# Kernel optimization log

Measured on AMD Instinct MI355X. Metric: run time of the kernel, lower is better.

## Reference

```python
import jax, jax.numpy as jnp
import numpy as np

N_NODES = 100_000
N_INC = 400_000
N_EDGES = 20_000
N_GRAPHS = 512
N_SEQ = 16
SEQ_LEN = 32
F_IN = 128
HIDDEN = 256
HEADS = 4
OUT = HIDDEN // HEADS  # 64 per head, concat -> HIDDEN
RNN_H = 256
OUT_DIM = 128
NEG_SLOPE = 0.2


def setup_inputs() -> dict:
    key = jax.random.key(0)
    ks = jax.random.split(key, 20)
    p = lambda i, shape: jax.random.normal(ks[i], shape, jnp.float32) * 0.05
    return {
        "x": jax.random.normal(ks[0], (N_NODES, F_IN), jnp.float32),
        "he_node": jax.random.randint(ks[1], (N_INC,), 0, N_NODES),
        "he_edge": jax.random.randint(ks[2], (N_INC,), 0, N_EDGES),
        "batch": jnp.sort(jax.random.randint(ks[3], (N_NODES,), 0, N_GRAPHS)),
        "w_lin": p(4, (F_IN, HIDDEN)),
        "att": p(5, (HEADS, 2 * OUT)),
        "bias": p(6, (HIDDEN,)),
        "w_ih0": p(7, (2, 4 * RNN_H, HIDDEN)),
        "w_hh0": p(8, (2, 4 * RNN_H, RNN_H)),
        "b_ih0": p(9, (2, 4 * RNN_H)),
        "b_hh0": p(10, (2, 4 * RNN_H)),
        "w_ih1": p(11, (2, 4 * RNN_H, 2 * RNN_H)),
        "w_hh1": p(12, (2, 4 * RNN_H, RNN_H)),
        "b_ih1": p(13, (2, 4 * RNN_H)),
        "b_hh1": p(14, (2, 4 * RNN_H)),
        "w_causal": p(15, (2 * RNN_H, HIDDEN)),
        "b_causal": p(16, (HIDDEN,)),
        "w_link": p(17, (HIDDEN, OUT_DIM)),
        "b_link": p(18, (OUT_DIM,)),
    }


def _segment_softmax(logits, seg, num_segments):
    m = jax.ops.segment_max(logits, seg, num_segments)
    m = jnp.where(jnp.isfinite(m), m, 0.0)
    e = jnp.exp(logits - m[seg])
    s = jax.ops.segment_sum(e, seg, num_segments)
    return e / jnp.maximum(s[seg], 1e-16)


def hypergraph_conv(x, he_node, he_edge, w_lin, att, bias):
    # PyG HypergraphConv, use_attention=True, attention_mode='node'.
    xh = (x @ w_lin).reshape(-1, HEADS, OUT)  # [N,H,O]
    ones_inc = jnp.ones((N_INC,), x.dtype)
    cnt_e = jax.ops.segment_sum(ones_inc, he_edge, N_EDGES)  # hyperedge sizes
    # hyperedge_attr = mean of incident raw node features, then shared lin
    eattr = jax.ops.segment_sum(x[he_node], he_edge, N_EDGES) / jnp.maximum(cnt_e, 1.0)[:, None]
    eh = (eattr @ w_lin).reshape(-1, HEADS, OUT)  # [M,H,O]
    x_i = xh[he_node]  # [E,H,O]
    e_j = eh[he_edge]  # [E,H,O]
    alpha = jnp.einsum("ehd,hd->eh", jnp.concatenate([x_i, e_j], axis=-1), att)
    alpha = jax.nn.leaky_relu(alpha, NEG_SLOPE)
    alpha = _segment_softmax(alpha, he_edge, N_EDGES)  # softmax within each hyperedge
    Binv = jnp.where(cnt_e > 0, 1.0 / cnt_e, 0.0)  # hyperedge degree norm
    deg = jax.ops.segment_sum(ones_inc, he_node, N_NODES)
    Dinv = jnp.where(deg > 0, 1.0 / deg, 0.0)  # node degree norm
    # node -> hyperedge, then hyperedge -> node, attention applied both hops
    out_e = Binv[:, None, None] * jax.ops.segment_sum(alpha[:, :, None] * x_i, he_edge, N_EDGES)
    out_n = Dinv[:, None, None] * jax.ops.segment_sum(alpha[:, :, None] * out_e[he_edge], he_node, N_NODES)
    return out_n.reshape(-1, HIDDEN) + bias


def _lstm_dir(xs, w_ih, w_hh, b_ih, b_hh, reverse):
    # xs: [T,B,I]; torch gate order i,f,g,o
    B = xs.shape[1]
    H = w_hh.shape[1]
    def step(carry, x_t):
        h, c = carry
        g = x_t @ w_ih.T + h @ w_hh.T + b_ih + b_hh
        i, f, gg, o = jnp.split(g, 4, axis=-1)
        c = jax.nn.sigmoid(f) * c + jax.nn.sigmoid(i) * jnp.tanh(gg)
        h = jax.nn.sigmoid(o) * jnp.tanh(c)
        return (h, c), h
    h0 = jnp.zeros((B, H), xs.dtype)
    _, hs = jax.lax.scan(step, (h0, h0), xs, reverse=reverse)
    return hs


def bilstm(x_seq, w_ih, w_hh, b_ih, b_hh):
    xs = jnp.swapaxes(x_seq, 0, 1)  # [T,B,I]
    fwd = _lstm_dir(xs, w_ih[0], w_hh[0], b_ih[0], b_hh[0], False)
    bwd = _lstm_dir(xs, w_ih[1], w_hh[1], b_ih[1], b_hh[1], True)
    return jnp.swapaxes(jnp.concatenate([fwd, bwd], axis=-1), 0, 1)


def reference(x, he_node, he_edge, batch, w_lin, att, bias,
              w_ih0, w_hh0, b_ih0, b_hh0, w_ih1, w_hh1, b_ih1, b_hh1,
              w_causal, b_causal, w_link, b_link):
    h = jax.nn.relu(hypergraph_conv(x, he_node, he_edge, w_lin, att, bias))  # [N,HIDDEN]
    cnt_g = jax.ops.segment_sum(jnp.ones((N_NODES,), h.dtype), batch, N_GRAPHS)
    pooled = jax.ops.segment_sum(h, batch, N_GRAPHS) / jnp.maximum(cnt_g, 1.0)[:, None]
    seq = pooled.reshape(N_SEQ, SEQ_LEN, HIDDEN)  # equal-length sequences of graphs
    l1 = bilstm(seq, w_ih0, w_hh0, b_ih0, b_hh0)   # [S,T,2*RNN_H]
    l2 = bilstm(l1, w_ih1, w_hh1, b_ih1, b_hh1)
    causal = jax.nn.relu(l2 @ w_causal + b_causal)
    return jax.nn.sigmoid(causal @ w_link + b_link)  # [S,T,OUT_DIM]
```

## Files before the change

### kernel.cpp

```cpp
#include <hip/hip_runtime.h>
#include <math.h>

#define N_NODES  100000
#define N_INC    400000
#define N_EDGES  20000
#define N_GRAPHS 512
#define F_IN     128
#define HID      256
#define RNN_H    256
#define ODIM     128

__global__ void k_count(const int* __restrict__ he_node, const int* __restrict__ he_edge,
                        int* __restrict__ cnt_e, int* __restrict__ deg) {
  int i = blockIdx.x * 256 + threadIdx.x;
  if (i >= N_INC) return;
  atomicAdd(&cnt_e[he_edge[i]], 1);
  atomicAdd(&deg[he_node[i]], 1);
}

__global__ __launch_bounds__(1024)
void k_scan(const int* __restrict__ cnt, int* __restrict__ start, int n) {
  __shared__ int part[1024];
  int tid = threadIdx.x;
  int chunk = (n + 1023) / 1024;
  int lo = tid * chunk; if (lo > n) lo = n;
  int hi = lo + chunk;  if (hi > n) hi = n;
  int s = 0;
  for (int i = lo; i < hi; ++i) s += cnt[i];
  part[tid] = s;
  __syncthreads();
  for (int off = 1; off < 1024; off <<= 1) {
    int v = (tid >= off) ? part[tid - off] : 0;
    __syncthreads();
    part[tid] += v;
    __syncthreads();
  }
  int run = (tid == 0) ? 0 : part[tid - 1];
  for (int i = lo; i < hi; ++i) { start[i] = run; run += cnt[i]; }
  if (tid == 1023) start[n] = part[1023];
}

__global__ void k_fill(const int* __restrict__ he_node, const int* __restrict__ he_edge,
                       const int* __restrict__ e_start, const int* __restrict__ n_start,
                       int* __restrict__ cur_e, int* __restrict__ cur_n,
                       int* __restrict__ e_idx, int* __restrict__ n_idx) {
  int i = blockIdx.x * 256 + threadIdx.x;
  if (i >= N_INC) return;
  int e = he_edge[i]; int p = atomicAdd(&cur_e[e], 1); e_idx[e_start[e] + p] = i;
  int nn = he_node[i]; int q = atomicAdd(&cur_n[nn], 1); n_idx[n_start[nn] + q] = i;
}

__global__ void k_transpose(const float* __restrict__ in, float* __restrict__ out,
                            int rows, int cols) {
  int idx = blockIdx.x * 256 + threadIdx.x;
  if (idx >= rows * cols) return;
  int r = idx / cols, c = idx - r * cols;
  out[c * rows + r] = in[idx];
}

template<int TT, int TR>
__global__ __launch_bounds__(256)
void k_gemm(const float* __restrict__ A, const float* __restrict__ WT,
            float* __restrict__ C, int M, int N, int K,
            const float* __restrict__ bias1, const float* __restrict__ bias2,
            int act, int remap) {
  __shared__ float As[TT][64];
  __shared__ float Ws[TT][64];
  const int m0 = blockIdx.y * TT, n0 = blockIdx.x * TT;
  const int tid = threadIdx.x;
  const int tc = tid & 15, tr = tid >> 4;
  float acc[TR][TR];
#pragma unroll
  for (int r = 0; r < TR; ++r)
#pragma unroll
    for (int c = 0; c < TR; ++c) acc[r][c] = 0.f;

  for (int kc = 0; kc < K; kc += 64) {
    for (int it = tid; it < TT * 16; it += 256) {
      int r = it >> 4, c4 = it & 15;
      int sw = ((c4 ^ (r >> 3)) & 15) << 2;
      int row = m0 + r;
      float4 v = {0.f, 0.f, 0.f, 0.f};
      if (row < M) v = *(const float4*)&A[(size_t)row * K + kc + c4 * 4];
      *(float4*)&As[r][sw] = v;
      float4 wv = *(const float4*)&WT[(size_t)(n0 + r) * K + kc + c4 * 4];
      *(float4*)&Ws[r][sw] = wv;
    }
    __syncthreads();
#pragma unroll 4
    for (int k4 = 0; k4 < 16; ++k4) {
      float4 wv[TR], av[TR];
#pragma unroll
      for (int c = 0; c < TR; ++c) {
        int rw = tc * TR + c;
        wv[c] = *(const float4*)&Ws[rw][((k4 ^ (rw >> 3)) & 15) << 2];
      }
#pragma unroll
      for (int r = 0; r < TR; ++r) {
        int ra = tr * TR + r;
        av[r] = *(const float4*)&As[ra][((k4 ^ (ra >> 3)) & 15) << 2];
      }
#pragma unroll
      for (int r = 0; r < TR; ++r)
#pragma unroll
        for (int c = 0; c < TR; ++c)
          acc[r][c] += av[r].x * wv[c].x + av[r].y * wv[c].y +
                       av[r].z * wv[c].z + av[r].w * wv[c].w;
    }
    __syncthreads();
  }

#pragma unroll
  for (int r = 0; r < TR; ++r) {
    int row = m0 + tr * TR + r;
    if (row >= M) continue;
    int orow = remap ? ((row & 15) * 32 + (row >> 4)) : row;
#pragma unroll
    for (int c4 = 0; c4 < TR; c4 += 4) {
      float4 o;
      float* op = &o.x;
#pragma unroll
      for (int c = 0; c < 4; ++c) {
        int col = n0 + tc * TR + c4 + c;
        float v = acc[r][c4 + c] +
                  (bias1 ? bias1[col] : 0.f) + (bias2 ? bias2[col] : 0.f);
        if (act == 1) v = fmaxf(v, 0.f);
        else if (act == 2) v = 1.f / (1.f + expf(-v));
        op[c] = v;
      }
      *(float4*)&C[(size_t)orow * N + n0 + tc * TR + c4] = o;
    }
  }
}

__global__ __launch_bounds__(256)
void k_eattr(const float* __restrict__ x, const int* __restrict__ he_node,
             const int* __restrict__ e_start, const int* __restrict__ e_idx,
             float* __restrict__ eattr) {
  int m = blockIdx.x * 4 + (threadIdx.x >> 6);
  if (m >= N_EDGES) return;
  int lane = threadIdx.x & 63;
  int c4 = lane & 31, jp = lane >> 5;
  int begin = e_start[m], end = e_start[m + 1];
  float4 acc = {0.f, 0.f, 0.f, 0.f};
  for (int j = begin + jp; j < end; j += 2) {
    float4 v = *(const float4*)&x[(size_t)he_node[e_idx[j]] * F_IN + c4 * 4];
    acc.x += v.x; acc.y += v.y; acc.z += v.z; acc.w += v.w;
  }
  acc.x += __shfl_xor(acc.x, 32); acc.y += __shfl_xor(acc.y, 32);
  acc.z += __shfl_xor(acc.z, 32); acc.w += __shfl_xor(acc.w, 32);
  if (jp == 0) {
    float inv = 1.f / fmaxf((float)(end - begin), 1.f);
    float4 o = {acc.x * inv, acc.y * inv, acc.z * inv, acc.w * inv};
    *(float4*)&eattr[(size_t)m * F_IN + c4 * 4] = o;
  }
}

__global__ __launch_bounds__(256)
void k_dot(const float* __restrict__ X, const float* __restrict__ att,
           float* __restrict__ s, int half, int nrows) {
  int row = blockIdx.x * 4 + (threadIdx.x >> 6);
  if (row >= nrows) return;
  int lane = threadIdx.x & 63;
  int h = lane >> 4;
  float4 v = *(const float4*)&X[(size_t)row * HID + lane * 4];
  float4 a = *(const float4*)&att[h * 128 + half * 64 + (lane & 15) * 4];
  float p = v.x * a.x + v.y * a.y + v.z * a.z + v.w * a.w;
  p += __shfl_xor(p, 1); p += __shfl_xor(p, 2);
  p += __shfl_xor(p, 4); p += __shfl_xor(p, 8);
  if ((lane & 15) == 0) s[(size_t)row * 4 + h] = p;
}

__global__ void k_logit(const int* __restrict__ he_node, const int* __restrict__ he_edge,
                        const float* __restrict__ s_n, const float* __restrict__ s_e,
                        float* __restrict__ alpha) {
  int i = blockIdx.x * 256 + threadIdx.x;
  if (i >= N_INC) return;
  float4 a = *(const float4*)&s_n[(size_t)he_node[i] * 4];
  float4 b = *(const float4*)&s_e[(size_t)he_edge[i] * 4];
  float4 o;
  o.x = a.x + b.x; o.y = a.y + b.y; o.z = a.z + b.z; o.w = a.w + b.w;
  o.x = o.x > 0.f ? o.x : 0.2f * o.x;
  o.y = o.y > 0.f ? o.y : 0.2f * o.y;
  o.z = o.z > 0.f ? o.z : 0.2f * o.z;
  o.w = o.w > 0.f ? o.w : 0.2f * o.w;
  *(float4*)&alpha[(size_t)i * 4] = o;
}

__global__ __launch_bounds__(256)
void k_softmax(const int* __restrict__ e_start, const int* __restrict__ e_idx,
               float* __restrict__ alpha) {
  int m = blockIdx.x * 4 + (threadIdx.x >> 6);
  if (m >= N_EDGES) return;
  int lane = threadIdx.x & 63;
  int begin = e_start[m], end = e_start[m + 1];
  int cnt = end - begin;
  if (cnt == 0) return;
  int nch = (cnt + 63) >> 6;
  float mx[4] = {-1e30f, -1e30f, -1e30f, -1e30f};
  for (int ch = 0; ch < nch; ++ch) {
    int j = begin + ch * 64 + lane;
    if (j < end) {
      float4 a = *(const float4*)&alpha[(size_t)e_idx[j] * 4];
      mx[0] = fmaxf(mx[0], a.x); mx[1] = fmaxf(mx[1], a.y);
      mx[2] = fmaxf(mx[2], a.z); mx[3] = fmaxf(mx[3], a.w);
    }
  }
#pragma unroll
  for (int h = 0; h < 4; ++h)
    for (int off = 32; off; off >>= 1) mx[h] = fmaxf(mx[h], __shfl_xor(mx[h], off));
  float s[4] = {0.f, 0.f, 0.f, 0.f};
  for (int ch = 0; ch < nch; ++ch) {
    int j = begin + ch * 64 + lane;
    if (j < end) {
      int i = e_idx[j];
      float4 a = *(const float4*)&alpha[(size_t)i * 4];
      a.x = expf(a.x - mx[0]); a.y = expf(a.y - mx[1]);
      a.z = expf(a.z - mx[2]); a.w = expf(a.w - mx[3]);
      *(float4*)&alpha[(size_t)i * 4] = a;
      s[0] += a.x; s[1] += a.y; s[2] += a.z; s[3] += a.w;
    }
  }
#pragma unroll
  for (int h = 0; h < 4; ++h) {
    for (int off = 32; off; off >>= 1) s[h] += __shfl_xor(s[h], off);
    s[h] = 1.f / fmaxf(s[h], 1e-16f);
  }
  for (int ch = 0; ch < nch; ++ch) {
    int j = begin + ch * 64 + lane;
    if (j < end) {
      int i = e_idx[j];
      float4 a = *(const float4*)&alpha[(size_t)i * 4];
      a.x *= s[0]; a.y *= s[1]; a.z *= s[2]; a.w *= s[3];
      *(float4*)&alpha[(size_t)i * 4] = a;
    }
  }
}

__global__ __launch_bounds__(256)
void k_out_e(const float* __restrict__ xh, const float* __restrict__ alpha,
             const int* __restrict__ e_start, const int* __restrict__ e_idx,
             const int* __restrict__ he_node, float* __restrict__ out_e) {
  int m = blockIdx.x * 4 + (threadIdx.x >> 6);
  if (m >= N_EDGES) return;
  int lane = threadIdx.x & 63, h = lane >> 4;
  int begin = e_start[m], end = e_start[m + 1];
  float4 acc = {0.f, 0.f, 0.f, 0.f};
  for (int j = begin; j < end; ++j) {
    int i = e_idx[j];
    float a = alpha[(size_t)i * 4 + h];
    float4 v = *(const float4*)&xh[(size_t)he_node[i] * HID + lane * 4];
    acc.x += a * v.x; acc.y += a * v.y; acc.z += a * v.z; acc.w += a * v.w;
  }
  float bi = (end > begin) ? 1.f / (float)(end - begin) : 0.f;
  float4 o = {acc.x * bi, acc.y * bi, acc.z * bi, acc.w * bi};
  *(float4*)&out_e[(size_t)m * HID + lane * 4] = o;
}

__global__ __launch_bounds__(256)
void k_out_n(const float* __restrict__ out_e, const float* __restrict__ alpha,
             const int* __restrict__ n_start, const int* __restrict__ n_idx,
             const int* __restrict__ he_edge, const float* __restrict__ bias,
             float* __restrict__ hout) {
  int n = blockIdx.x * 4 + (threadIdx.x >> 6);
  if (n >= N_NODES) return;
  int lane = threadIdx.x & 63, h = lane >> 4;
  int begin = n_start[n], end = n_start[n + 1];
  float4 acc = {0.f, 0.f, 0.f, 0.f};
  for (int j = begin; j < end; ++j) {
    int i = n_idx[j];
    float a = alpha[(size_t)i * 4 + h];
    float4 v = *(const float4*)&out_e[(size_t)he_edge[i] * HID + lane * 4];
    acc.x += a * v.x; acc.y += a * v.y; acc.z += a * v.z; acc.w += a * v.w;
  }
  float di = (end > begin) ? 1.f / (float)(end - begin) : 0.f;
  float4 bb = *(const float4*)&bias[lane * 4];
  float4 o;
  o.x = fmaxf(acc.x * di + bb.x, 0.f);
  o.y = fmaxf(acc.y * di + bb.y, 0.f);
  o.z = fmaxf(acc.z * di + bb.z, 0.f);
  o.w = fmaxf(acc.w * di + bb.w, 0.f);
  *(float4*)&hout[(size_t)n * HID + lane * 4] = o;
}

__global__ void k_gstart(const int* __restrict__ batch, int* __restrict__ gs) {
  int g = blockIdx.x * 256 + threadIdx.x;
  if (g > N_GRAPHS) return;
  int lo = 0, hi = N_NODES;
  while (lo < hi) { int mid = (lo + hi) >> 1; if (batch[mid] < g) lo = mid + 1; else hi = mid; }
  gs[g] = lo;
}

__global__ __launch_bounds__(256)
void k_pool(const float* __restrict__ h, const int* __restrict__ gs,
            float* __restrict__ pooled) {
  __shared__ float4 part[4][64];
  int g = blockIdx.x, tid = threadIdx.x;
  int rs = tid >> 6, c4 = tid & 63;
  int begin = gs[g], end = gs[g + 1];
  float4 acc = {0.f, 0.f, 0.f, 0.f};
  for (int n = begin + rs; n < end; n += 4) {
    float4 v = *(const float4*)&h[(size_t)n * HID + c4 * 4];
    acc.x += v.x; acc.y += v.y; acc.z += v.z; acc.w += v.w;
  }
  part[rs][c4] = acc;
  __syncthreads();
  if (rs == 0) {
    float4 a = part[0][c4], b = part[1][c4], c = part[2][c4], d = part[3][c4];
    float inv = 1.f / fmaxf((float)(end - begin), 1.f);
    float4 o = {(a.x + b.x + c.x + d.x) * inv, (a.y + b.y + c.y + d.y) * inv,
                (a.z + b.z + c.z + d.z) * inv, (a.w + b.w + c.w + d.w) * inv};
    *(float4*)&pooled[(size_t)g * HID + c4 * 4] = o;
  }
}

__global__ __launch_bounds__(256)
void k_lstm2(const float* __restrict__ xg, const float* __restrict__ w_hh,
             float* __restrict__ out, float* __restrict__ hbuf,
             int* __restrict__ stamp, int rst, int rsb) {
  __shared__ float4 ws4[64][64];
  __shared__ float4 hs[16 * 64];
  const int dir = blockIdx.x >> 4, q = blockIdx.x & 15;
  const int tid = threadIdx.x;
  const int l = tid & 63, w = tid >> 6;
  const int ks = l & 3, rg = l >> 2;

  for (int it = tid; it < 4096; it += 256) {
    int row = it >> 6, c4 = it & 63;
    int g = row >> 4, r = row & 15;
    float4 v = *(const float4*)&w_hh[((size_t)dir * 1024 + g * 256 + q * 16 + r) * 256 + c4 * 4];
    ws4[row][c4 ^ ((c4 >> 4) & 3) ^ (r & 7)] = v;
  }
  __syncthreads();

  float cst[4] = {0.f, 0.f, 0.f, 0.f};
  for (int t = 0; t < 32; ++t) {
    const int te = dir ? (31 - t) : t;
    float xr[4][4];
#pragma unroll
    for (int lb = 0; lb < 4; ++lb) {
      const float* xp = &xg[(size_t)((w * 4 + lb) * rsb + te * rst) * 2048 + dir * 1024 + q * 16 + rg];
      xr[0][lb] = xp[0];
      xr[1][lb] = xp[256];
      xr[2][lb] = xp[512];
      xr[3][lb] = xp[768];
    }
    if (t > 0) {
      for (;;) {
        int sv = t;
        if (l < 16)
          sv = __hip_atomic_load(&stamp[dir * 16 + l], __ATOMIC_RELAXED, __HIP_MEMORY_SCOPE_AGENT);
        if (__all(sv >= t)) break;
        __builtin_amdgcn_s_sleep(1);
      }
    }
    const float* hprev = hbuf + ((size_t)(t & 1) * 2 + dir) * 16 * 256;
    float4 hv0, hv1, hv2, hv3;
    {
      const float* a0 = hprev + (0 * 256 + tid) * 4;
      const float* a1 = hprev + (1 * 256 + tid) * 4;
      const float* a2 = hprev + (2 * 256 + tid) * 4;
      const float* a3 = hprev + (3 * 256 + tid) * 4;
      asm volatile(
        "global_load_dwordx4 %0, %4, off sc0 sc1\n"
        "global_load_dwordx4 %1, %5, off sc0 sc1\n"
        "global_load_dwordx4 %2, %6, off sc0 sc1\n"
        "global_load_dwordx4 %3, %7, off sc0 sc1\n"
        "s_waitcnt vmcnt(0)"
        : "=&v"(hv0), "=&v"(hv1), "=&v"(hv2), "=&v"(hv3)
        : "v"(a0), "v"(a1), "v"(a2), "v"(a3)
        : "memory");
    }
#pragma unroll
    for (int i = 0; i < 4; ++i) {
      int idx = i * 256 + tid;
      int b = idx >> 6, cc = idx & 63;
      float4 hv = (i == 0) ? hv0 : (i == 1) ? hv1 : (i == 2) ? hv2 : hv3;
      hs[b * 64 + (cc ^ ((cc >> 4) & 3))] = hv;
    }
    __syncthreads();

    float acc[4][4];
#pragma unroll
    for (int g = 0; g < 4; ++g)
#pragma unroll
      for (int lb = 0; lb < 4; ++lb) acc[g][lb] = 0.f;
#pragma unroll
    for (int j = 0; j < 16; ++j) {
      int col = ks * 16 + j;
      int u = col ^ ((col >> 4) & 3);
      float4 h4[4];
#pragma unroll
      for (int lb = 0; lb < 4; ++lb)
        h4[lb] = hs[(w * 4 + lb) * 64 + u];
      int csw = col ^ ks ^ (rg & 7);
#pragma unroll
      for (int g = 0; g < 4; ++g) {
        float4 wv = ws4[g * 16 + rg][csw];
#pragma unroll
        for (int lb = 0; lb < 4; ++lb)
          acc[g][lb] += wv.x * h4[lb].x + wv.y * h4[lb].y + wv.z * h4[lb].z + wv.w * h4[lb].w;
      }
    }
#pragma unroll
    for (int g = 0; g < 4; ++g)
#pragma unroll
      for (int lb = 0; lb < 4; ++lb) {
        float v = acc[g][lb];
        v += __shfl_xor(v, 1);
        v += __shfl_xor(v, 2);
        acc[g][lb] = v;
      }
    float hv[4];
#pragma unroll
    for (int lb = 0; lb < 4; ++lb) {
      float gi = acc[0][lb] + xr[0][lb];
      float gf = acc[1][lb] + xr[1][lb];
      float gg = acc[2][lb] + xr[2][lb];
      float go = acc[3][lb] + xr[3][lb];
      gi = 1.f / (1.f + expf(-gi));
      gf = 1.f / (1.f + expf(-gf));
      gg = tanhf(gg);
      go = 1.f / (1.f + expf(-go));
      cst[lb] = gf * cst[lb] + gi * gg;
      hv[lb] = go * tanhf(cst[lb]);
    }
    float* hnext = hbuf + ((size_t)((t + 1) & 1) * 2 + dir) * 16 * 256;
    if (ks == 0) {
#pragma unroll
      for (int lb = 0; lb < 4; ++lb) {
        int b = w * 4 + lb;
        __hip_atomic_store(&hnext[b * 256 + q * 16 + rg], hv[lb],
                           __ATOMIC_RELAXED, __HIP_MEMORY_SCOPE_AGENT);
        out[((size_t)te * 16 + b) * 512 + dir * 256 + q * 16 + rg] = hv[lb];
      }
    }
    if (t < 31) {
      __syncthreads();
      if (tid == 0)
        __hip_atomic_store(&stamp[dir * 16 + q], t + 1,
                           __ATOMIC_RELAXED, __HIP_MEMORY_SCOPE_AGENT);
    }
  }
}

extern "C" void kernel_launch(void* const* d_in, const int* in_sizes, int n_in,
                              void* d_out, int out_size, void* d_ws, size_t ws_size,
                              hipStream_t stream) {
  const float* x        = (const float*)d_in[0];
  const int*   he_node  = (const int*)d_in[1];
  const int*   he_edge  = (const int*)d_in[2];
  const int*   batch    = (const int*)d_in[3];
  const float* w_lin    = (const float*)d_in[4];
  const float* att      = (const float*)d_in[5];
  const float* bias     = (const float*)d_in[6];
  const float* w_ih0    = (const float*)d_in[7];
  const float* w_hh0    = (const float*)d_in[8];
  const float* b_ih0    = (const float*)d_in[9];
  const float* b_hh0    = (const float*)d_in[10];
  const float* w_ih1    = (const float*)d_in[11];
  const float* w_hh1    = (const float*)d_in[12];
  const float* b_ih1    = (const float*)d_in[13];
  const float* b_hh1    = (const float*)d_in[14];
  const float* w_causal = (const float*)d_in[15];
  const float* b_causal = (const float*)d_in[16];
  const float* w_link   = (const float*)d_in[17];
  const float* b_link   = (const float*)d_in[18];
  float* out = (float*)d_out;

  char* ws = (char*)d_ws;
  size_t off = 0;
  auto alloc = [&](size_t bytes) -> void* {
    void* p = ws + off;
    off = (off + bytes + 255) & ~(size_t)255;
    return p;
  };
  float* xh      = (float*)alloc((size_t)N_NODES * HID * 4);
  float* eattr   = (float*)alloc((size_t)N_EDGES * F_IN * 4);
  float* eh      = (float*)alloc((size_t)N_EDGES * HID * 4);
  float* alpha   = (float*)alloc((size_t)N_INC * 4 * 4);
  float* out_e   = (float*)alloc((size_t)N_EDGES * HID * 4);
  float* s_n     = (float*)alloc((size_t)N_NODES * 4 * 4);
  float* s_e     = (float*)alloc((size_t)N_EDGES * 4 * 4);
  int*   cnt_e   = (int*)alloc(N_EDGES * 4);
  int*   deg     = (int*)alloc(N_NODES * 4);
  int*   e_start = (int*)alloc((N_EDGES + 1) * 4);
  int*   n_start = (int*)alloc((N_NODES + 1) * 4);
  int*   cur_e   = (int*)alloc(N_EDGES * 4);
  int*   cur_n   = (int*)alloc(N_NODES * 4);
  int*   e_idx   = (int*)alloc(N_INC * 4);
  int*   n_idx   = (int*)alloc(N_INC * 4);
  int*   gstart  = (int*)alloc((N_GRAPHS + 1) * 4);
  float* pooled  = (float*)alloc((size_t)N_GRAPHS * HID * 4);
  float* wlinT   = (float*)alloc((size_t)HID * F_IN * 4);
  float* wcT     = (float*)alloc((size_t)HID * 512 * 4);
  float* wlkT    = (float*)alloc((size_t)ODIM * HID * 4);
  float* xg1     = (float*)alloc((size_t)512 * 2048 * 4);
  float* xg2     = (float*)alloc((size_t)512 * 2048 * 4);
  float* l1      = (float*)alloc((size_t)512 * 512 * 4);
  float* l2      = (float*)alloc((size_t)512 * 512 * 4);
  float* causal  = (float*)alloc((size_t)512 * HID * 4);
  float* hbuf    = (float*)alloc((size_t)2 * 2 * 2 * 16 * 256 * 4);
  int*   lcnt    = (int*)alloc(2 * 32 * 4);

  (void)hipMemsetAsync(cnt_e, 0, N_EDGES * 4, stream);
  (void)hipMemsetAsync(deg,   0, N_NODES * 4, stream);
  (void)hipMemsetAsync(cur_e, 0, N_EDGES * 4, stream);
  (void)hipMemsetAsync(cur_n, 0, N_NODES * 4, stream);
  (void)hipMemsetAsync(hbuf,  0, (size_t)2 * 2 * 2 * 16 * 256 * 4, stream);
  (void)hipMemsetAsync(lcnt,  0, 2 * 32 * 4, stream);

  k_count<<<(N_INC + 255) / 256, 256, 0, stream>>>(he_node, he_edge, cnt_e, deg);
  k_scan<<<1, 1024, 0, stream>>>(cnt_e, e_start, N_EDGES);
  k_scan<<<1, 1024, 0, stream>>>(deg, n_start, N_NODES);
  k_fill<<<(N_INC + 255) / 256, 256, 0, stream>>>(he_node, he_edge, e_start, n_start,
                                                  cur_e, cur_n, e_idx, n_idx);
  k_gstart<<<(N_GRAPHS + 1 + 255) / 256, 256, 0, stream>>>(batch, gstart);
  k_transpose<<<(F_IN * HID + 255) / 256, 256, 0, stream>>>(w_lin, wlinT, F_IN, HID);
  k_transpose<<<(512 * HID + 255) / 256, 256, 0, stream>>>(w_causal, wcT, 512, HID);
  k_transpose<<<(HID * ODIM + 255) / 256, 256, 0, stream>>>(w_link, wlkT, HID, ODIM);

  k_gemm<128, 8><<<dim3(HID / 128, (N_NODES + 127) / 128), 256, 0, stream>>>(
      x, wlinT, xh, N_NODES, HID, F_IN, nullptr, nullptr, 0, 0);
  k_eattr<<<N_EDGES / 4, 256, 0, stream>>>(x, he_node, e_start, e_idx, eattr);
  k_gemm<128, 8><<<dim3(HID / 128, (N_EDGES + 127) / 128), 256, 0, stream>>>(
      eattr, wlinT, eh, N_EDGES, HID, F_IN, nullptr, nullptr, 0, 0);
  k_dot<<<N_NODES / 4, 256, 0, stream>>>(xh, att, s_n, 0, N_NODES);
  k_dot<<<N_EDGES / 4, 256, 0, stream>>>(eh, att, s_e, 1, N_EDGES);
  k_logit<<<(N_INC + 255) / 256, 256, 0, stream>>>(he_node, he_edge, s_n, s_e, alpha);
  k_softmax<<<N_EDGES / 4, 256, 0, stream>>>(e_start, e_idx, alpha);
  k_out_e<<<N_EDGES / 4, 256, 0, stream>>>(xh, alpha, e_start, e_idx, he_node, out_e);
  k_out_n<<<N_NODES / 4, 256, 0, stream>>>(out_e, alpha, n_start, n_idx, he_edge, bias, xh);
  k_pool<<<N_GRAPHS, 256, 0, stream>>>(xh, gstart, pooled);

  k_gemm<64, 4><<<dim3(2048 / 64, 512 / 64), 256, 0, stream>>>(
      pooled, w_ih0, xg1, 512, 2048, HID, b_ih0, b_hh0, 0, 0);
  k_lstm2<<<32, 256, 0, stream>>>(xg1, w_hh0, l1, hbuf, lcnt, 1, 32);
  k_gemm<64, 4><<<dim3(2048 / 64, 512 / 64), 256, 0, stream>>>(
      l1, w_ih1, xg2, 512, 2048, 512, b_ih1, b_hh1, 0, 0);
  k_lstm2<<<32, 256, 0, stream>>>(xg2, w_hh1, l2, hbuf + 2 * 2 * 16 * 256, lcnt + 32, 16, 1);
  k_gemm<64, 4><<<dim3(HID / 64, 512 / 64), 256, 0, stream>>>(
      l2, wcT, causal, 512, HID, 512, b_causal, nullptr, 1, 0);
  k_gemm<64, 4><<<dim3(ODIM / 64, 512 / 64), 256, 0, stream>>>(
      causal, wlkT, out, 512, ODIM, HID, b_link, nullptr, 2, 1);
  (void)in_sizes; (void)n_in; (void)out_size; (void)ws_size;
}
```

Before: 1.452 ms.

## Replace LSTM step counters with sentinel-filled per-timestep hidden-state slots

The cross-block LSTM recurrence previously waited on per-block stamp counters and then read a double-buffered hidden state. It now gives every timestep its own hidden-state slot, pre-filled with a sentinel bit pattern, and each block polls the data itself until no sentinel values remain. This removes the stamp store, the extra barrier before it and the separate counter polling, cutting one round trip of latency per step. In exchange it needs a larger workspace plus a big memset, and it would break if a real hidden value ever matched the sentinel pattern.

Result: no change. 1.472 ms (+1.3%).

```diff
diff --git a/kernel.cpp b/kernel.cpp
--- a/kernel.cpp
+++ b/kernel.cpp
@@ -9,6 +9,8 @@
 #define HID      256
 #define RNN_H    256
 #define ODIM     128
+#define SENT     0x7F7F7F7Fu
+#define LSLOT    (33 * 2 * 16 * 256)
 
 __global__ void k_count(const int* __restrict__ he_node, const int* __restrict__ he_edge,
                         int* __restrict__ cnt_e, int* __restrict__ deg) {
@@ -317,7 +319,7 @@
 __global__ __launch_bounds__(256)
 void k_lstm2(const float* __restrict__ xg, const float* __restrict__ w_hh,
              float* __restrict__ out, float* __restrict__ hbuf,
-             int* __restrict__ stamp, int rst, int rsb) {
+             int rst, int rsb) {
   __shared__ float4 ws4[64][64];
   __shared__ float4 hs[16 * 64];
   const int dir = blockIdx.x >> 4, q = blockIdx.x & 15;
@@ -345,31 +347,34 @@
       xr[2][lb] = xp[512];
       xr[3][lb] = xp[768];
     }
-    if (t > 0) {
-      for (;;) {
-        int sv = t;
-        if (l < 16)
-          sv = __hip_atomic_load(&stamp[dir * 16 + l], __ATOMIC_RELAXED, __HIP_MEMORY_SCOPE_AGENT);
-        if (__all(sv >= t)) break;
-        __builtin_amdgcn_s_sleep(1);
-      }
-    }
-    const float* hprev = hbuf + ((size_t)(t & 1) * 2 + dir) * 16 * 256;
+    const float* hprev = hbuf + ((size_t)t * 2 + dir) * 16 * 256;
     float4 hv0, hv1, hv2, hv3;
     {
       const float* a0 = hprev + (0 * 256 + tid) * 4;
       const float* a1 = hprev + (1 * 256 + tid) * 4;
       const float* a2 = hprev + (2 * 256 + tid) * 4;
       const float* a3 = hprev + (3 * 256 + tid) * 4;
-      asm volatile(
-        "global_load_dwordx4 %0, %4, off sc0 sc1\n"
-        "global_load_dwordx4 %1, %5, off sc0 sc1\n"
-        "global_load_dwordx4 %2, %6, off sc0 sc1\n"
-        "global_load_dwordx4 %3, %7, off sc0 sc1\n"
-        "s_waitcnt vmcnt(0)"
-        : "=&v"(hv0), "=&v"(hv1), "=&v"(hv2), "=&v"(hv3)
-        : "v"(a0), "v"(a1), "v"(a2), "v"(a3)
-        : "memory");
+      for (;;) {
+        asm volatile(
+          "global_load_dwordx4 %0, %4, off sc0 sc1\n"
+          "global_load_dwordx4 %1, %5, off sc0 sc1\n"
+          "global_load_dwordx4 %2, %6, off sc0 sc1\n"
+          "global_load_dwordx4 %3, %7, off sc0 sc1\n"
+          "s_waitcnt vmcnt(0)"
+          : "=&v"(hv0), "=&v"(hv1), "=&v"(hv2), "=&v"(hv3)
+          : "v"(a0), "v"(a1), "v"(a2), "v"(a3)
+          : "memory");
+        bool bad = (__float_as_uint(hv0.x) == SENT) | (__float_as_uint(hv0.y) == SENT) |
+                   (__float_as_uint(hv0.z) == SENT) | (__float_as_uint(hv0.w) == SENT) |
+                   (__float_as_uint(hv1.x) == SENT) | (__float_as_uint(hv1.y) == SENT) |
+                   (__float_as_uint(hv1.z) == SENT) | (__float_as_uint(hv1.w) == SENT) |
+                   (__float_as_uint(hv2.x) == SENT) | (__float_as_uint(hv2.y) == SENT) |
+                   (__float_as_uint(hv2.z) == SENT) | (__float_as_uint(hv2.w) == SENT) |
+                   (__float_as_uint(hv3.x) == SENT) | (__float_as_uint(hv3.y) == SENT) |
+                   (__float_as_uint(hv3.z) == SENT) | (__float_as_uint(hv3.w) == SENT);
+        if (!bad) break;
+        __builtin_amdgcn_s_sleep(1);
+      }
     }
 #pragma unroll
     for (int i = 0; i < 4; ++i) {
@@ -402,6 +407,8 @@
           acc[g][lb] += wv.x * h4[lb].x + wv.y * h4[lb].y + wv.z * h4[lb].z + wv.w * h4[lb].w;
       }
     }
+    __syncthreads();
+
 #pragma unroll
     for (int g = 0; g < 4; ++g)
 #pragma unroll
@@ -425,21 +432,16 @@
       cst[lb] = gf * cst[lb] + gi * gg;
       hv[lb] = go * tanhf(cst[lb]);
     }
-    float* hnext = hbuf + ((size_t)((t + 1) & 1) * 2 + dir) * 16 * 256;
+    float* hnext = hbuf + ((size_t)(t + 1) * 2 + dir) * 16 * 256;
     if (ks == 0) {
 #pragma unroll
       for (int lb = 0; lb < 4; ++lb) {
         int b = w * 4 + lb;
-        __hip_atomic_store(&hnext[b * 256 + q * 16 + rg], hv[lb],
-                           __ATOMIC_RELAXED, __HIP_MEMORY_SCOPE_AGENT);
+        if (t < 31)
+          __hip_atomic_store(&hnext[b * 256 + q * 16 + rg], hv[lb],
+                             __ATOMIC_RELAXED, __HIP_MEMORY_SCOPE_AGENT);
         out[((size_t)te * 16 + b) * 512 + dir * 256 + q * 16 + rg] = hv[lb];
       }
-    }
-    if (t < 31) {
-      __syncthreads();
-      if (tid == 0)
-        __hip_atomic_store(&stamp[dir * 16 + q], t + 1,
-                           __ATOMIC_RELAXED, __HIP_MEMORY_SCOPE_AGENT);
     }
   }
 }
@@ -500,15 +502,15 @@
   float* l1      = (float*)alloc((size_t)512 * 512 * 4);
   float* l2      = (float*)alloc((size_t)512 * 512 * 4);
   float* causal  = (float*)alloc((size_t)512 * HID * 4);
-  float* hbuf    = (float*)alloc((size_t)2 * 2 * 2 * 16 * 256 * 4);
-  int*   lcnt    = (int*)alloc(2 * 32 * 4);
+  float* hbuf    = (float*)alloc((size_t)2 * LSLOT * 4);
 
   (void)hipMemsetAsync(cnt_e, 0, N_EDGES * 4, stream);
   (void)hipMemsetAsync(deg,   0, N_NODES * 4, stream);
   (void)hipMemsetAsync(cur_e, 0, N_EDGES * 4, stream);
   (void)hipMemsetAsync(cur_n, 0, N_NODES * 4, stream);
-  (void)hipMemsetAsync(hbuf,  0, (size_t)2 * 2 * 2 * 16 * 256 * 4, stream);
-  (void)hipMemsetAsync(lcnt,  0, 2 * 32 * 4, stream);
+  (void)hipMemsetAsync(hbuf,  0x7F, (size_t)2 * LSLOT * 4, stream);
+  (void)hipMemsetAsync(hbuf,  0, 2 * 16 * 256 * 4, stream);
+  (void)hipMemsetAsync(hbuf + LSLOT, 0, 2 * 16 * 256 * 4, stream);
 
   k_count<<<(N_INC + 255) / 256, 256, 0, stream>>>(he_node, he_edge, cnt_e, deg);
   k_scan<<<1, 1024, 0, stream>>>(cnt_e, e_start, N_EDGES);
@@ -535,10 +537,10 @@
 
   k_gemm<64, 4><<<dim3(2048 / 64, 512 / 64), 256, 0, stream>>>(
       pooled, w_ih0, xg1, 512, 2048, HID, b_ih0, b_hh0, 0, 0);
-  k_lstm2<<<32, 256, 0, stream>>>(xg1, w_hh0, l1, hbuf, lcnt, 1, 32);
+  k_lstm2<<<32, 256, 0, stream>>>(xg1, w_hh0, l1, hbuf, 1, 32);
   k_gemm<64, 4><<<dim3(2048 / 64, 512 / 64), 256, 0, stream>>>(
       l1, w_ih1, xg2, 512, 2048, 512, b_ih1, b_hh1, 0, 0);
-  k_lstm2<<<32, 256, 0, stream>>>(xg2, w_hh1, l2, hbuf + 2 * 2 * 16 * 256, lcnt + 32, 16, 1);
+  k_lstm2<<<32, 256, 0, stream>>>(xg2, w_hh1, l2, hbuf + LSLOT, 16, 1);
   k_gemm<64, 4><<<dim3(HID / 64, 512 / 64), 256, 0, stream>>>(
       l2, wcT, causal, 512, HID, 512, b_causal, nullptr, 1, 0);
   k_gemm<64, 4><<<dim3(ODIM / 64, 512 / 64), 256, 0, stream>>>(
```
